# Kernel tuning notes

Measured on AMD Instinct MI355X. Metric: run time of the kernel, lower is better.

The kernel has to match this reference:

```python
import jax, jax.numpy as jnp
import numpy as np

N, E = 50000, 800000
IN, HID, H, OUT = 128, 32, 4, 32
NEG_SLOPE = 0.2


def _gatv2_layer(x, edge_index, Wl, bl, Wr, br, att, bias, heads, ch, concat):
    """One GATv2Conv layer (PyG semantics: add self-loops, lin_l on source,
    lin_r on target, e = att . leaky_relu(gl_src + gr_dst), segment softmax
    over incoming edges of each target, scatter-add weighted source messages)."""
    n = x.shape[0]
    loop = jnp.arange(n)
    src = jnp.concatenate([edge_index[0], loop])
    dst = jnp.concatenate([edge_index[1], loop])

    gl = (x @ Wl + bl).reshape(n, heads, ch)   # source transform [N,H,C]
    gr = (x @ Wr + br).reshape(n, heads, ch)   # target transform [N,H,C]

    m = jax.nn.leaky_relu(gl[src] + gr[dst], NEG_SLOPE)   # [E+N,H,C]
    e = jnp.einsum('ehc,hc->eh', m, att)                   # [E+N,H]

    # numerically stable segment softmax over dst
    emax = jax.lax.stop_gradient(jax.ops.segment_max(e, dst, num_segments=n))
    ex = jnp.exp(e - emax[dst])
    denom = jax.ops.segment_sum(ex, dst, num_segments=n)
    alpha = ex / denom[dst]                                # [E+N,H]

    out = jax.ops.segment_sum(alpha[:, :, None] * gl[src], dst, num_segments=n)  # [N,H,C]
    out = out.reshape(n, heads * ch) if concat else out.mean(axis=1)
    return out + bias


def setup_inputs() -> dict:
    key = jax.random.key(0)
    ks = jax.random.split(key, 16)
    s = 0.05
    return {
        'x': jax.random.normal(ks[0], (N, IN), dtype=jnp.float32),
        'edge_index': jax.random.randint(ks[1], (2, E), 0, N, dtype=jnp.int32),
        # layer 1: IN -> HID, H heads, concat
        'Wl1': jax.random.normal(ks[2], (IN, H * HID), dtype=jnp.float32) * s,
        'bl1': jnp.zeros((H * HID,), dtype=jnp.float32),
        'Wr1': jax.random.normal(ks[3], (IN, H * HID), dtype=jnp.float32) * s,
        'br1': jnp.zeros((H * HID,), dtype=jnp.float32),
        'att1': jax.random.normal(ks[4], (H, HID), dtype=jnp.float32) * s,
        'bias1': jnp.zeros((H * HID,), dtype=jnp.float32),
        # layer 2: H*HID -> OUT, 1 head, no concat
        'Wl2': jax.random.normal(ks[5], (H * HID, OUT), dtype=jnp.float32) * s,
        'bl2': jnp.zeros((OUT,), dtype=jnp.float32),
        'Wr2': jax.random.normal(ks[6], (H * HID, OUT), dtype=jnp.float32) * s,
        'br2': jnp.zeros((OUT,), dtype=jnp.float32),
        'att2': jax.random.normal(ks[7], (1, OUT), dtype=jnp.float32) * s,
        'bias2': jnp.zeros((OUT,), dtype=jnp.float32),
    }


def reference(x, edge_index, Wl1, bl1, Wr1, br1, att1, bias1,
              Wl2, bl2, Wr2, br2, att2, bias2):
    h = jax.nn.elu(_gatv2_layer(x, edge_index, Wl1, bl1, Wr1, br1, att1, bias1, H, HID, True))
    # dropout inactive in eval mode
    return _gatv2_layer(h, edge_index, Wl2, bl2, Wr2, br2, att2, bias2, 1, OUT, False)
```

## Files before the change

kernel.cpp:

```cpp
#include <hip/hip_runtime.h>

#define NNODES 50000
#define NEDGES 800000
#define ETOT   (NNODES + NEDGES)
#define NEG 0.2f
#define BKTS 196
#define P1E 4096
#define NP1 ((ETOT + P1E - 1) / P1E)

typedef unsigned short ushort_t;
typedef unsigned int uint_t;
typedef __attribute__((ext_vector_type(8))) short short8;
typedef __attribute__((ext_vector_type(4))) float f32x4;

__device__ __forceinline__ ushort_t f2bf(float f) {
  uint_t u = __float_as_uint(f);
  u += 0x7FFFu + ((u >> 16) & 1u);
  return (ushort_t)(u >> 16);
}
__device__ __forceinline__ float bf2f(ushort_t h) {
  return __uint_as_float((uint_t)h << 16);
}

__global__ __launch_bounds__(256) void coarse_hist(const int* __restrict__ ei,
                                                   int* __restrict__ pcnt) {
  __shared__ int c[BKTS];
  for (int i = threadIdx.x; i < BKTS; i += 256) c[i] = 0;
  __syncthreads();
  int e0 = blockIdx.x * P1E;
#pragma unroll
  for (int t = 0; t < P1E / 256; ++t) {
    int i = e0 + t * 256 + (int)threadIdx.x;
    if (i < ETOT) {
      int dst = (i < NEDGES) ? ei[NEDGES + i] : (i - NEDGES);
      atomicAdd(&c[dst >> 8], 1);
    }
  }
  __syncthreads();
  for (int i = threadIdx.x; i < BKTS; i += 256)
    pcnt[i * NP1 + blockIdx.x] = c[i];
}

__global__ __launch_bounds__(64) void coarse_scan(const int* __restrict__ pcnt,
                                                  int* __restrict__ goffArr,
                                                  int* __restrict__ tot) {
  int b = blockIdx.x;
  int lane = threadIdx.x;
  int carry = 0;
  for (int k0 = 0; k0 < NP1; k0 += 64) {
    int k = k0 + lane;
    int v = (k < NP1) ? pcnt[b * NP1 + k] : 0;
    int s = v;
    for (int off = 1; off < 64; off <<= 1) {
      int u = __shfl_up(s, off);
      if (lane >= off) s += u;
    }
    if (k < NP1) goffArr[b * NP1 + k] = carry + s - v;
    carry += __shfl(s, 63);
  }
  if (lane == 0) tot[b] = carry;
}

__global__ __launch_bounds__(256) void bucket_scan(const int* __restrict__ tot,
                                                   int* __restrict__ bucketStart,
                                                   int* __restrict__ rowptr) {
  if (threadIdx.x == 0) {
    int r = 0;
    for (int i = 0; i < BKTS; ++i) { bucketStart[i] = r; r += tot[i]; }
    bucketStart[BKTS] = r;
    rowptr[NNODES] = ETOT;
  }
}

__global__ __launch_bounds__(256) void bin_phase1(const int* __restrict__ ei,
                                                  const int* __restrict__ bucketStart,
                                                  const int* __restrict__ goffArr,
                                                  uint_t* __restrict__ binned) {
  __shared__ int cnt[BKTS], pref[BKTS], fillL[BKTS];
  __shared__ uint_t stage[P1E];
  int e0 = blockIdx.x * P1E;
  for (int i = threadIdx.x; i < BKTS; i += 256) { cnt[i] = 0; fillL[i] = 0; }
  __syncthreads();
  uint_t mypk[P1E / 256];
  int mybkt[P1E / 256];
#pragma unroll
  for (int t = 0; t < P1E / 256; ++t) {
    int i = e0 + t * 256 + (int)threadIdx.x;
    if (i < ETOT) {
      int dst = (i < NEDGES) ? ei[NEDGES + i] : (i - NEDGES);
      int src = (i < NEDGES) ? ei[i] : dst;
      int b = dst >> 8;
      mypk[t] = (uint_t)src | ((uint_t)(dst & 255) << 16) | ((uint_t)b << 24);
      mybkt[t] = b;
      atomicAdd(&cnt[b], 1);
    } else mybkt[t] = -1;
  }
  __syncthreads();
  if (threadIdx.x == 0) {
    int r = 0;
    for (int b = 0; b < BKTS; ++b) { pref[b] = r; r += cnt[b]; }
  }
  __syncthreads();
#pragma unroll
  for (int t = 0; t < P1E / 256; ++t) {
    if (mybkt[t] >= 0) {
      int p = pref[mybkt[t]] + atomicAdd(&fillL[mybkt[t]], 1);
      stage[p] = mypk[t];
    }
  }
  __syncthreads();
  int total = (e0 + P1E <= ETOT) ? P1E : (ETOT - e0);
  for (int j = threadIdx.x; j < total; j += 256) {
    uint_t pk = stage[j];
    int b = pk >> 24;
    binned[bucketStart[b] + goffArr[b * NP1 + blockIdx.x] + (j - pref[b])] = pk;
  }
}

__global__ __launch_bounds__(256) void bin_phase2(const uint_t* __restrict__ binned,
                                                  const int* __restrict__ bucketStart,
                                                  int* __restrict__ rowptr,
                                                  int* __restrict__ csrc) {
  __shared__ int cnt[256], pref[256], fillL[256];
  __shared__ int outS[8192];
  int b = blockIdx.x;
  int base = bucketStart[b];
  int cntAll = bucketStart[b + 1] - base;
  cnt[threadIdx.x] = 0; fillL[threadIdx.x] = 0;
  __syncthreads();
  for (int j = threadIdx.x; j < cntAll; j += 256)
    atomicAdd(&cnt[(binned[base + j] >> 16) & 255], 1);
  __syncthreads();
  if (threadIdx.x == 0) {
    int r = 0;
    for (int i = 0; i < 256; ++i) { pref[i] = r; r += cnt[i]; }
  }
  __syncthreads();
  int node = b * 256 + (int)threadIdx.x;
  if (node < NNODES) rowptr[node] = base + pref[threadIdx.x];
  for (int j = threadIdx.x; j < cntAll; j += 256) {
    uint_t pk = binned[base + j];
    int d = (pk >> 16) & 255;
    int p = pref[d] + atomicAdd(&fillL[d], 1);
    outS[p] = (int)(pk & 0xFFFF);
  }
  __syncthreads();
  for (int j = threadIdx.x; j < cntAll; j += 256)
    csrc[base + j] = outS[j];
}

__global__ __launch_bounds__(256) void prep_w(const float* __restrict__ Wl1,
                                              const float* __restrict__ Wr1,
                                              ushort_t* __restrict__ WtHi,
                                              ushort_t* __restrict__ WtLo) {
  int k = blockIdx.x;
  int n = threadIdx.x;
  float w = (n < 128) ? Wl1[k * 128 + n] : Wr1[k * 128 + (n - 128)];
  ushort_t h = f2bf(w);
  WtHi[n * 128 + k] = h;
  WtLo[n * 128 + k] = f2bf(w - bf2f(h));
}

__global__ __launch_bounds__(256) void gemm1_mfma(
    const float* __restrict__ x,
    const ushort_t* __restrict__ WtHi, const ushort_t* __restrict__ WtLo,
    const float* __restrict__ bl1, const float* __restrict__ br1,
    ushort_t* __restrict__ gl1, ushort_t* __restrict__ gr1) {
  constexpr int LDA = 132;
  __shared__ __align__(16) char smem[32 * 260 * 4];
  ushort_t (*Ahi)[LDA] = (ushort_t(*)[LDA])smem;
  ushort_t (*Alo)[LDA] = (ushort_t(*)[LDA])(smem + 32 * LDA * 2);
  float (*Cs)[260] = (float(*)[260])smem;
  int m0 = blockIdx.x * 32;
  int tid = threadIdx.x;
#pragma unroll
  for (int i = 0; i < 4; ++i) {
    int it = i * 256 + tid;
    int row = it >> 5, c4 = it & 31;
    int gm = m0 + row;
    float4 v = (gm < NNODES) ? *(const float4*)&x[(size_t)gm * 128 + 4 * c4]
                             : make_float4(0.f, 0.f, 0.f, 0.f);
    ushort_t h0 = f2bf(v.x), h1 = f2bf(v.y), h2 = f2bf(v.z), h3 = f2bf(v.w);
    ushort_t l0 = f2bf(v.x - bf2f(h0)), l1 = f2bf(v.y - bf2f(h1));
    ushort_t l2 = f2bf(v.z - bf2f(h2)), l3 = f2bf(v.w - bf2f(h3));
    uint2 ph, pl;
    ph.x = (uint_t)h0 | ((uint_t)h1 << 16); ph.y = (uint_t)h2 | ((uint_t)h3 << 16);
    pl.x = (uint_t)l0 | ((uint_t)l1 << 16); pl.y = (uint_t)l2 | ((uint_t)l3 << 16);
    *(uint2*)&Ahi[row][4 * c4] = ph;
    *(uint2*)&Alo[row][4 * c4] = pl;
  }
  __syncthreads();
  int wave = tid >> 6, lane = tid & 63;
  int quad = lane >> 4, nl = lane & 15;
  int nb = wave * 64;
  f32x4 acc[2][4];
#pragma unroll
  for (int tm = 0; tm < 2; ++tm)
#pragma unroll
    for (int tn = 0; tn < 4; ++tn) acc[tm][tn] = (f32x4){0.f, 0.f, 0.f, 0.f};

#pragma unroll
  for (int kc = 0; kc < 4; ++kc) {
    int klane = kc * 32 + quad * 8;
    short8 ah[2], al[2], bh[4], bl[4];
#pragma unroll
    for (int tm = 0; tm < 2; ++tm) {
      ah[tm] = *(const short8*)&Ahi[16 * tm + nl][klane];
      al[tm] = *(const short8*)&Alo[16 * tm + nl][klane];
    }
#pragma unroll
    for (int tn = 0; tn < 4; ++tn) {
      size_t wo = (size_t)(nb + 16 * tn + nl) * 128 + klane;
      bh[tn] = *(const short8*)&WtHi[wo];
      bl[tn] = *(const short8*)&WtLo[wo];
    }
#pragma unroll
    for (int tm = 0; tm < 2; ++tm)
#pragma unroll
      for (int tn = 0; tn < 4; ++tn) {
        acc[tm][tn] = __builtin_amdgcn_mfma_f32_16x16x32_bf16(ah[tm], bh[tn], acc[tm][tn], 0, 0, 0);
        acc[tm][tn] = __builtin_amdgcn_mfma_f32_16x16x32_bf16(ah[tm], bl[tn], acc[tm][tn], 0, 0, 0);
        acc[tm][tn] = __builtin_amdgcn_mfma_f32_16x16x32_bf16(al[tm], bh[tn], acc[tm][tn], 0, 0, 0);
      }
  }
  float bb[4];
#pragma unroll
  for (int tn = 0; tn < 4; ++tn) {
    int n = nb + 16 * tn + nl;
    bb[tn] = (n < 128) ? bl1[n] : br1[n - 128];
  }
  __syncthreads();
#pragma unroll
  for (int tm = 0; tm < 2; ++tm)
#pragma unroll
    for (int tn = 0; tn < 4; ++tn)
#pragma unroll
      for (int r = 0; r < 4; ++r)
        Cs[16 * tm + 4 * quad + r][nb + 16 * tn + nl] = acc[tm][tn][r] + bb[tn];
  __syncthreads();
#pragma unroll
  for (int i = 0; i < 2; ++i) {
    int it = i * 256 + tid;
    int row = it >> 4, oc = (it & 15) * 8;
    int gm = m0 + row;
    if (gm < NNODES) {
      uint4 pk;
      pk.x = (uint_t)f2bf(Cs[row][oc + 0]) | ((uint_t)f2bf(Cs[row][oc + 1]) << 16);
      pk.y = (uint_t)f2bf(Cs[row][oc + 2]) | ((uint_t)f2bf(Cs[row][oc + 3]) << 16);
      pk.z = (uint_t)f2bf(Cs[row][oc + 4]) | ((uint_t)f2bf(Cs[row][oc + 5]) << 16);
      pk.w = (uint_t)f2bf(Cs[row][oc + 6]) | ((uint_t)f2bf(Cs[row][oc + 7]) << 16);
      *(uint4*)&gl1[(size_t)gm * 128 + oc] = pk;
    }
  }
#pragma unroll
  for (int i = 0; i < 2; ++i) {
    int it = i * 256 + tid;
    int row = it >> 4, oc = (it & 15) * 8;
    int gm = m0 + row;
    if (gm < NNODES) {
      uint4 pk;
      pk.x = (uint_t)f2bf(Cs[row][128 + oc + 0]) | ((uint_t)f2bf(Cs[row][128 + oc + 1]) << 16);
      pk.y = (uint_t)f2bf(Cs[row][128 + oc + 2]) | ((uint_t)f2bf(Cs[row][128 + oc + 3]) << 16);
      pk.z = (uint_t)f2bf(Cs[row][128 + oc + 4]) | ((uint_t)f2bf(Cs[row][128 + oc + 5]) << 16);
      pk.w = (uint_t)f2bf(Cs[row][128 + oc + 6]) | ((uint_t)f2bf(Cs[row][128 + oc + 7]) << 16);
      *(uint4*)&gr1[(size_t)gm * 128 + oc] = pk;
    }
  }
}

__global__ __launch_bounds__(128) void gemm2_tile(
    const ushort_t* __restrict__ A,
    const float* __restrict__ W1, const float* __restrict__ b1,
    const float* __restrict__ W2, const float* __restrict__ b2,
    ushort_t* __restrict__ G1, ushort_t* __restrict__ G2) {
  constexpr int K = 128, KC = 32, BM = 128, BN = 64, MCOLS = 32, NT = 128;
  constexpr int LDA = BM + 4;
  __shared__ float AsT[KC][LDA];
  __shared__ float Ws[KC][BN];
  int row0 = blockIdx.x * BM;
  int tid = threadIdx.x;
  int tx = tid % (BN / 8), ty = tid / (BN / 8);
  float acc[8][8];
#pragma unroll
  for (int i = 0; i < 8; ++i)
#pragma unroll
    for (int j = 0; j < 8; ++j) acc[i][j] = 0.f;

  for (int kc = 0; kc < K; kc += KC) {
#pragma unroll
    for (int item = tid; item < BM * (KC / 4); item += NT) {
      int r = item >> 3, f4 = item & 7;
      int grow = row0 + r;
      uint2 u = (grow < NNODES)
          ? *(const uint2*)&A[(size_t)grow * K + kc + 4 * f4]
          : make_uint2(0u, 0u);
      AsT[4 * f4 + 0][r] = __uint_as_float(u.x << 16);
      AsT[4 * f4 + 1][r] = __uint_as_float(u.x & 0xffff0000u);
      AsT[4 * f4 + 2][r] = __uint_as_float(u.y << 16);
      AsT[4 * f4 + 3][r] = __uint_as_float(u.y & 0xffff0000u);
    }
#pragma unroll
    for (int item = tid; item < KC * (BN / 4); item += NT) {
      int k = item / (BN / 4), c4 = item % (BN / 4);
      int ccat = 4 * c4;
      const float* src = (ccat < MCOLS)
          ? &W1[(size_t)(kc + k) * MCOLS + ccat]
          : &W2[(size_t)(kc + k) * MCOLS + ccat - MCOLS];
      *(float4*)&Ws[k][4 * c4] = *(const float4*)src;
    }
    __syncthreads();
#pragma unroll 8
    for (int k = 0; k < KC; ++k) {
      float4 a0 = *(const float4*)&AsT[k][4 * ty];
      float4 a1 = *(const float4*)&AsT[k][BM / 2 + 4 * ty];
      float4 w0 = *(const float4*)&Ws[k][4 * tx];
      float4 w1 = *(const float4*)&Ws[k][BN / 2 + 4 * tx];
      float av[8] = {a0.x, a0.y, a0.z, a0.w, a1.x, a1.y, a1.z, a1.w};
      float wv[8] = {w0.x, w0.y, w0.z, w0.w, w1.x, w1.y, w1.z, w1.w};
#pragma unroll
      for (int i = 0; i < 8; ++i)
#pragma unroll
        for (int j = 0; j < 8; ++j) acc[i][j] = fmaf(av[i], wv[j], acc[i][j]);
    }
    __syncthreads();
  }
#pragma unroll
  for (int i = 0; i < 8; ++i) {
    int row = row0 + (i < 4 ? 4 * ty + i : BM / 2 + 4 * ty + (i - 4));
    if (row >= NNODES) continue;
#pragma unroll
    for (int jj = 0; jj < 2; ++jj) {
      int ccat = (jj == 0 ? 4 * tx : BN / 2 + 4 * tx);
      float o0 = acc[i][4 * jj + 0], o1 = acc[i][4 * jj + 1];
      float o2 = acc[i][4 * jj + 2], o3 = acc[i][4 * jj + 3];
      if (ccat < MCOLS) {
        float4 bb = *(const float4*)&b1[ccat];
        uint2 pk;
        pk.x = (uint_t)f2bf(o0 + bb.x) | ((uint_t)f2bf(o1 + bb.y) << 16);
        pk.y = (uint_t)f2bf(o2 + bb.z) | ((uint_t)f2bf(o3 + bb.w) << 16);
        *(uint2*)&G1[(size_t)row * MCOLS + ccat] = pk;
      } else {
        int c = ccat - MCOLS;
        float4 bb = *(const float4*)&b2[c];
        uint2 pk;
        pk.x = (uint_t)f2bf(o0 + bb.x) | ((uint_t)f2bf(o1 + bb.y) << 16);
        pk.y = (uint_t)f2bf(o2 + bb.z) | ((uint_t)f2bf(o3 + bb.w) << 16);
        *(uint2*)&G2[(size_t)row * MCOLS + c] = pk;
      }
    }
  }
}

__global__ __launch_bounds__(256) void gat1_edge(const int* __restrict__ rowptr,
                          const int* __restrict__ csrc,
                          const ushort_t* __restrict__ glb,
                          const ushort_t* __restrict__ grb,
                          const float* __restrict__ att, const float* __restrict__ bias,
                          ushort_t* __restrict__ hout) {
  int node = blockIdx.x * 4 + (threadIdx.x >> 6);
  if (node >= NNODES) return;
  int lane = threadIdx.x & 63;
  int eslot = lane >> 4;
  int q = lane & 15;
  int c8 = q * 8;
  float4 av0 = *(const float4*)(att + c8);
  float4 av1 = *(const float4*)(att + c8 + 4);
  uint4 ug = *(const uint4*)(grb + (size_t)node * 128 + c8);
  float4 gr0, gr1v;
  gr0.x = __uint_as_float(ug.x << 16);  gr0.y = __uint_as_float(ug.x & 0xffff0000u);
  gr0.z = __uint_as_float(ug.y << 16);  gr0.w = __uint_as_float(ug.y & 0xffff0000u);
  gr1v.x = __uint_as_float(ug.z << 16); gr1v.y = __uint_as_float(ug.z & 0xffff0000u);
  gr1v.z = __uint_as_float(ug.w << 16); gr1v.w = __uint_as_float(ug.w & 0xffff0000u);
  int start = rowptr[node], end = rowptr[node + 1];
  float denom = 0.f;
  float4 A0 = make_float4(0.f, 0.f, 0.f, 0.f);
  float4 A1 = make_float4(0.f, 0.f, 0.f, 0.f);
  for (int b = start; b < end; b += 64) {
    int nb = end - b; if (nb > 64) nb = 64;
    int sidx = (lane < nb) ? csrc[b + lane] : 0;
    for (int j = 0; j < nb; j += 4) {
      bool pv = (j + eslot) < nb;
      int s = __shfl(sidx, j + eslot);
      uint4 up = *(const uint4*)(glb + (size_t)s * 128 + c8);
      float4 g0, g1;
      g0.x = __uint_as_float(up.x << 16);
      g0.y = __uint_as_float(up.x & 0xffff0000u);
      g0.z = __uint_as_float(up.y << 16);
      g0.w = __uint_as_float(up.y & 0xffff0000u);
      g1.x = __uint_as_float(up.z << 16);
      g1.y = __uint_as_float(up.z & 0xffff0000u);
      g1.z = __uint_as_float(up.w << 16);
      g1.w = __uint_as_float(up.w & 0xffff0000u);
      float t, v;
      t = g0.x + gr0.x; t = fmaxf(t, NEG * t); v = av0.x * t;
      t = g0.y + gr0.y; t = fmaxf(t, NEG * t); v = fmaf(av0.y, t, v);
      t = g0.z + gr0.z; t = fmaxf(t, NEG * t); v = fmaf(av0.z, t, v);
      t = g0.w + gr0.w; t = fmaxf(t, NEG * t); v = fmaf(av0.w, t, v);
      t = g1.x + gr1v.x; t = fmaxf(t, NEG * t); v = fmaf(av1.x, t, v);
      t = g1.y + gr1v.y; t = fmaxf(t, NEG * t); v = fmaf(av1.y, t, v);
      t = g1.z + gr1v.z; t = fmaxf(t, NEG * t); v = fmaf(av1.z, t, v);
      t = g1.w + gr1v.w; t = fmaxf(t, NEG * t); v = fmaf(av1.w, t, v);
      v += __shfl_xor(v, 1); v += __shfl_xor(v, 2);
      float ex = pv ? __expf(v) : 0.f;
      denom += ex;
      A0.x = fmaf(ex, g0.x, A0.x); A0.y = fmaf(ex, g0.y, A0.y);
      A0.z = fmaf(ex, g0.z, A0.z); A0.w = fmaf(ex, g0.w, A0.w);
      A1.x = fmaf(ex, g1.x, A1.x); A1.y = fmaf(ex, g1.y, A1.y);
      A1.z = fmaf(ex, g1.z, A1.z); A1.w = fmaf(ex, g1.w, A1.w);
    }
  }
  denom += __shfl_xor(denom, 16); denom += __shfl_xor(denom, 32);
  A0.x += __shfl_xor(A0.x, 16); A0.x += __shfl_xor(A0.x, 32);
  A0.y += __shfl_xor(A0.y, 16); A0.y += __shfl_xor(A0.y, 32);
  A0.z += __shfl_xor(A0.z, 16); A0.z += __shfl_xor(A0.z, 32);
  A0.w += __shfl_xor(A0.w, 16); A0.w += __shfl_xor(A0.w, 32);
  A1.x += __shfl_xor(A1.x, 16); A1.x += __shfl_xor(A1.x, 32);
  A1.y += __shfl_xor(A1.y, 16); A1.y += __shfl_xor(A1.y, 32);
  A1.z += __shfl_xor(A1.z, 16); A1.z += __shfl_xor(A1.z, 32);
  A1.w += __shfl_xor(A1.w, 16); A1.w += __shfl_xor(A1.w, 32);
  float inv = 1.f / denom;
  if (eslot == 0) {
    float4 bv = *(const float4*)(bias + c8);
    float o0 = A0.x * inv + bv.x, o1 = A0.y * inv + bv.y;
    float o2 = A0.z * inv + bv.z, o3 = A0.w * inv + bv.w;
    o0 = o0 > 0.f ? o0 : __expf(o0) - 1.f;
    o1 = o1 > 0.f ? o1 : __expf(o1) - 1.f;
    o2 = o2 > 0.f ? o2 : __expf(o2) - 1.f;
    o3 = o3 > 0.f ? o3 : __expf(o3) - 1.f;
    uint2 pk;
    pk.x = (uint_t)f2bf(o0) | ((uint_t)f2bf(o1) << 16);
    pk.y = (uint_t)f2bf(o2) | ((uint_t)f2bf(o3) << 16);
    *(uint2*)&hout[(size_t)node * 128 + c8] = pk;
  } else if (eslot == 1) {
    float4 bv = *(const float4*)(bias + c8 + 4);
    float o0 = A1.x * inv + bv.x, o1 = A1.y * inv + bv.y;
    float o2 = A1.z * inv + bv.z, o3 = A1.w * inv + bv.w;
    o0 = o0 > 0.f ? o0 : __expf(o0) - 1.f;
    o1 = o1 > 0.f ? o1 : __expf(o1) - 1.f;
    o2 = o2 > 0.f ? o2 : __expf(o2) - 1.f;
    o3 = o3 > 0.f ? o3 : __expf(o3) - 1.f;
    uint2 pk;
    pk.x = (uint_t)f2bf(o0) | ((uint_t)f2bf(o1) << 16);
    pk.y = (uint_t)f2bf(o2) | ((uint_t)f2bf(o3) << 16);
    *(uint2*)&hout[(size_t)node * 128 + c8 + 4] = pk;
  }
}

__global__ __launch_bounds__(256) void gat2_edge(const int* __restrict__ rowptr,
                          const int* __restrict__ csrc,
                          const ushort_t* __restrict__ gl, const ushort_t* __restrict__ gr,
                          const float* __restrict__ att, const float* __restrict__ bias,
                          float* __restrict__ out) {
  int node = blockIdx.x * 4 + (threadIdx.x >> 6);
  if (node >= NNODES) return;
  int lane = threadIdx.x & 63;
  int eslot = lane >> 3;
  int q = lane & 7;
  int c4 = q * 4;
  float4 avc = *(const float4*)(att + c4);
  uint2 ugr = *(const uint2*)(gr + (size_t)node * 32 + c4);
  float4 grd;
  grd.x = __uint_as_float(ugr.x << 16); grd.y = __uint_as_float(ugr.x & 0xffff0000u);
  grd.z = __uint_as_float(ugr.y << 16); grd.w = __uint_as_float(ugr.y & 0xffff0000u);
  int start = rowptr[node], end = rowptr[node + 1];
  float denom = 0.f;
  float4 A = make_float4(0.f, 0.f, 0.f, 0.f);
  for (int b = start; b < end; b += 64) {
    int nb = end - b; if (nb > 64) nb = 64;
    int sidx = (lane < nb) ? csrc[b + lane] : 0;
    for (int j = 0; j < nb; j += 8) {
      bool pv = (j + eslot) < nb;
      int s = __shfl(sidx, j + eslot);
      uint2 ug = *(const uint2*)(gl + (size_t)s * 32 + c4);
      float4 g;
      g.x = __uint_as_float(ug.x << 16); g.y = __uint_as_float(ug.x & 0xffff0000u);
      g.z = __uint_as_float(ug.y << 16); g.w = __uint_as_float(ug.y & 0xffff0000u);
      float t, v;
      t = g.x + grd.x; t = fmaxf(t, NEG * t); v = avc.x * t;
      t = g.y + grd.y; t = fmaxf(t, NEG * t); v = fmaf(avc.y, t, v);
      t = g.z + grd.z; t = fmaxf(t, NEG * t); v = fmaf(avc.z, t, v);
      t = g.w + grd.w; t = fmaxf(t, NEG * t); v = fmaf(avc.w, t, v);
      v += __shfl_xor(v, 1); v += __shfl_xor(v, 2); v += __shfl_xor(v, 4);
      float ex = pv ? __expf(v) : 0.f;
      denom += ex;
      A.x = fmaf(ex, g.x, A.x); A.y = fmaf(ex, g.y, A.y);
      A.z = fmaf(ex, g.z, A.z); A.w = fmaf(ex, g.w, A.w);
    }
  }
  denom += __shfl_xor(denom, 8); denom += __shfl_xor(denom, 16); denom += __shfl_xor(denom, 32);
  A.x += __shfl_xor(A.x, 8); A.x += __shfl_xor(A.x, 16); A.x += __shfl_xor(A.x, 32);
  A.y += __shfl_xor(A.y, 8); A.y += __shfl_xor(A.y, 16); A.y += __shfl_xor(A.y, 32);
  A.z += __shfl_xor(A.z, 8); A.z += __shfl_xor(A.z, 16); A.z += __shfl_xor(A.z, 32);
  A.w += __shfl_xor(A.w, 8); A.w += __shfl_xor(A.w, 16); A.w += __shfl_xor(A.w, 32);
  if (eslot == 0) {
    float4 bv = *(const float4*)(bias + c4);
    float inv = 1.f / denom;
    float4 o;
    o.x = A.x * inv + bv.x; o.y = A.y * inv + bv.y;
    o.z = A.z * inv + bv.z; o.w = A.w * inv + bv.w;
    *(float4*)(out + (size_t)node * 32 + c4) = o;
  }
}

extern "C" void kernel_launch(void* const* d_in, const int* in_sizes, int n_in,
                              void* d_out, int out_size, void* d_ws, size_t ws_size,
                              hipStream_t stream) {
  const float* x     = (const float*)d_in[0];
  const int*   ei    = (const int*)  d_in[1];
  const float* Wl1   = (const float*)d_in[2];
  const float* bl1   = (const float*)d_in[3];
  const float* Wr1   = (const float*)d_in[4];
  const float* br1   = (const float*)d_in[5];
  const float* att1  = (const float*)d_in[6];
  const float* bias1 = (const float*)d_in[7];
  const float* Wl2   = (const float*)d_in[8];
  const float* bl2   = (const float*)d_in[9];
  const float* Wr2   = (const float*)d_in[10];
  const float* br2   = (const float*)d_in[11];
  const float* att2  = (const float*)d_in[12];
  const float* bias2 = (const float*)d_in[13];
  float* out = (float*)d_out;

  char* w = (char*)d_ws;
  auto carve = [&](size_t bytes) {
    char* p = w;
    w += (bytes + 255) & ~(size_t)255;
    return p;
  };
  ushort_t* gl1 = (ushort_t*)carve((size_t)NNODES * 128 * 2);
  ushort_t* gr1 = (ushort_t*)carve((size_t)NNODES * 128 * 2);
  ushort_t* h   = (ushort_t*)carve((size_t)NNODES * 128 * 2);
  ushort_t* gl2 = (ushort_t*)carve((size_t)NNODES * 32 * 2);
  ushort_t* gr2 = (ushort_t*)carve((size_t)NNODES * 32 * 2);
  ushort_t* WtHi = (ushort_t*)carve((size_t)256 * 128 * 2);
  ushort_t* WtLo = (ushort_t*)carve((size_t)256 * 128 * 2);
  int* pcnt    = (int*)carve((size_t)NP1 * BKTS * 4);
  int* goffArr = (int*)carve((size_t)NP1 * BKTS * 4);
  int* tot     = (int*)carve((size_t)BKTS * 4);
  int* bucketStart = (int*)carve((size_t)(BKTS + 1) * 4);
  int* rowptr = (int*)carve((size_t)(NNODES + 1) * 4);
  uint_t* binned = (uint_t*)carve((size_t)ETOT * 4);
  int* csrc = (int*)carve((size_t)ETOT * 4);

  prep_w<<<128, 256, 0, stream>>>(Wl1, Wr1, WtHi, WtLo);
  coarse_hist<<<NP1, 256, 0, stream>>>(ei, pcnt);
  coarse_scan<<<BKTS, 64, 0, stream>>>(pcnt, goffArr, tot);
  bucket_scan<<<1, 256, 0, stream>>>(tot, bucketStart, rowptr);
  bin_phase1<<<NP1, 256, 0, stream>>>(ei, bucketStart, goffArr, binned);
  bin_phase2<<<BKTS, 256, 0, stream>>>(binned, bucketStart, rowptr, csrc);

  gemm1_mfma<<<(NNODES + 31) / 32, 256, 0, stream>>>(x, WtHi, WtLo, bl1, br1, gl1, gr1);
  gat1_edge<<<(NNODES + 3) / 4, 256, 0, stream>>>(rowptr, csrc, gl1, gr1, att1, bias1, h);
  gemm2_tile<<<(NNODES + 127) / 128, 128, 0, stream>>>(h, Wl2, bl2, Wr2, br2, gl2, gr2);
  gat2_edge<<<(NNODES + 3) / 4, 256, 0, stream>>>(rowptr, csrc, gl2, gr2, att2, bias2, out);
}
```

Baseline: 264.3 us.

## Prefetch next gather, rewrite leaky-relu algebraically, exp2, smaller blocks, warp-parallel bucket scan

The edge kernels now software-pipeline the gather of source features, issuing the load for the next group of edges before computing on the current one. The leaky-relu-then-dot is rewritten as a·(c6·t + c4·|t|) with log2(e) folded into the attention constants, so exp2 replaces exp. Reciprocal uses the hardware rcp and 32-bit byte offsets replace size_t index math. Block size drops to 128 threads (2 nodes per block), and the serial single-thread bucket scan becomes a wavefront shuffle scan. This adds register pressure and slightly lower-precision rcp/exp in exchange for hiding gather latency and trimming ALU work.

```diff
diff --git a/kernel.cpp b/kernel.cpp
--- a/kernel.cpp
+++ b/kernel.cpp
@@ -61,13 +61,24 @@
   if (lane == 0) tot[b] = carry;
 }
 
-__global__ __launch_bounds__(256) void bucket_scan(const int* __restrict__ tot,
-                                                   int* __restrict__ bucketStart,
-                                                   int* __restrict__ rowptr) {
-  if (threadIdx.x == 0) {
-    int r = 0;
-    for (int i = 0; i < BKTS; ++i) { bucketStart[i] = r; r += tot[i]; }
-    bucketStart[BKTS] = r;
+__global__ __launch_bounds__(64) void bucket_scan(const int* __restrict__ tot,
+                                                  int* __restrict__ bucketStart,
+                                                  int* __restrict__ rowptr) {
+  int lane = threadIdx.x;
+  int carry = 0;
+  for (int k0 = 0; k0 < BKTS; k0 += 64) {
+    int k = k0 + lane;
+    int v = (k < BKTS) ? tot[k] : 0;
+    int s = v;
+    for (int off = 1; off < 64; off <<= 1) {
+      int u = __shfl_up(s, off);
+      if (lane >= off) s += u;
+    }
+    if (k < BKTS) bucketStart[k] = carry + s - v;
+    carry += __shfl(s, 63);
+  }
+  if (lane == 0) {
+    bucketStart[BKTS] = carry;
     rowptr[NNODES] = ETOT;
   }
 }
@@ -351,20 +362,27 @@
   }
 }
 
-__global__ __launch_bounds__(256) void gat1_edge(const int* __restrict__ rowptr,
+__global__ __launch_bounds__(128) void gat1_edge(const int* __restrict__ rowptr,
                           const int* __restrict__ csrc,
                           const ushort_t* __restrict__ glb,
                           const ushort_t* __restrict__ grb,
                           const float* __restrict__ att, const float* __restrict__ bias,
                           ushort_t* __restrict__ hout) {
-  int node = blockIdx.x * 4 + (threadIdx.x >> 6);
+  int node = blockIdx.x * 2 + (threadIdx.x >> 6);
   if (node >= NNODES) return;
   int lane = threadIdx.x & 63;
   int eslot = lane >> 4;
   int q = lane & 15;
   int c8 = q * 8;
+  const float C6 = 0.8656170245333781f;
+  const float C4 = 0.5770780163555854f;
   float4 av0 = *(const float4*)(att + c8);
   float4 av1 = *(const float4*)(att + c8 + 4);
+  float4 a60, a61, a40, a41;
+  a60.x = C6 * av0.x; a60.y = C6 * av0.y; a60.z = C6 * av0.z; a60.w = C6 * av0.w;
+  a61.x = C6 * av1.x; a61.y = C6 * av1.y; a61.z = C6 * av1.z; a61.w = C6 * av1.w;
+  a40.x = C4 * av0.x; a40.y = C4 * av0.y; a40.z = C4 * av0.z; a40.w = C4 * av0.w;
+  a41.x = C4 * av1.x; a41.y = C4 * av1.y; a41.z = C4 * av1.z; a41.w = C4 * av1.w;
   uint4 ug = *(const uint4*)(grb + (size_t)node * 128 + c8);
   float4 gr0, gr1v;
   gr0.x = __uint_as_float(ug.x << 16);  gr0.y = __uint_as_float(ug.x & 0xffff0000u);
@@ -375,13 +393,19 @@
   float denom = 0.f;
   float4 A0 = make_float4(0.f, 0.f, 0.f, 0.f);
   float4 A1 = make_float4(0.f, 0.f, 0.f, 0.f);
+  const char* glc = (const char*)glb;
+  uint_t coff = (uint_t)(c8 * 2);
   for (int b = start; b < end; b += 64) {
     int nb = end - b; if (nb > 64) nb = 64;
     int sidx = (lane < nb) ? csrc[b + lane] : 0;
+    int s0 = __shfl(sidx, eslot);
+    uint4 up = *(const uint4*)(glc + (((uint_t)s0 << 8) + coff));
     for (int j = 0; j < nb; j += 4) {
       bool pv = (j + eslot) < nb;
-      int s = __shfl(sidx, j + eslot);
-      uint4 up = *(const uint4*)(glb + (size_t)s * 128 + c8);
+      int jn = j + 4 + eslot;
+      int jc = (jn < nb) ? jn : 0;
+      int sn = __shfl(sidx, jc);
+      uint4 upn = *(const uint4*)(glc + (((uint_t)sn << 8) + coff));
       float4 g0, g1;
       g0.x = __uint_as_float(up.x << 16);
       g0.y = __uint_as_float(up.x & 0xffff0000u);
@@ -392,21 +416,22 @@
       g1.z = __uint_as_float(up.w << 16);
       g1.w = __uint_as_float(up.w & 0xffff0000u);
       float t, v;
-      t = g0.x + gr0.x; t = fmaxf(t, NEG * t); v = av0.x * t;
-      t = g0.y + gr0.y; t = fmaxf(t, NEG * t); v = fmaf(av0.y, t, v);
-      t = g0.z + gr0.z; t = fmaxf(t, NEG * t); v = fmaf(av0.z, t, v);
-      t = g0.w + gr0.w; t = fmaxf(t, NEG * t); v = fmaf(av0.w, t, v);
-      t = g1.x + gr1v.x; t = fmaxf(t, NEG * t); v = fmaf(av1.x, t, v);
-      t = g1.y + gr1v.y; t = fmaxf(t, NEG * t); v = fmaf(av1.y, t, v);
-      t = g1.z + gr1v.z; t = fmaxf(t, NEG * t); v = fmaf(av1.z, t, v);
-      t = g1.w + gr1v.w; t = fmaxf(t, NEG * t); v = fmaf(av1.w, t, v);
+      t = g0.x + gr0.x;  v = fmaf(a40.x, fabsf(t), a60.x * t);
+      t = g0.y + gr0.y;  v = fmaf(a60.y, t, v); v = fmaf(a40.y, fabsf(t), v);
+      t = g0.z + gr0.z;  v = fmaf(a60.z, t, v); v = fmaf(a40.z, fabsf(t), v);
+      t = g0.w + gr0.w;  v = fmaf(a60.w, t, v); v = fmaf(a40.w, fabsf(t), v);
+      t = g1.x + gr1v.x; v = fmaf(a61.x, t, v); v = fmaf(a41.x, fabsf(t), v);
+      t = g1.y + gr1v.y; v = fmaf(a61.y, t, v); v = fmaf(a41.y, fabsf(t), v);
+      t = g1.z + gr1v.z; v = fmaf(a61.z, t, v); v = fmaf(a41.z, fabsf(t), v);
+      t = g1.w + gr1v.w; v = fmaf(a61.w, t, v); v = fmaf(a41.w, fabsf(t), v);
       v += __shfl_xor(v, 1); v += __shfl_xor(v, 2);
-      float ex = pv ? __expf(v) : 0.f;
+      float ex = pv ? exp2f(v) : 0.f;
       denom += ex;
       A0.x = fmaf(ex, g0.x, A0.x); A0.y = fmaf(ex, g0.y, A0.y);
       A0.z = fmaf(ex, g0.z, A0.z); A0.w = fmaf(ex, g0.w, A0.w);
       A1.x = fmaf(ex, g1.x, A1.x); A1.y = fmaf(ex, g1.y, A1.y);
       A1.z = fmaf(ex, g1.z, A1.z); A1.w = fmaf(ex, g1.w, A1.w);
+      up = upn;
     }
   }
   denom += __shfl_xor(denom, 16); denom += __shfl_xor(denom, 32);
@@ -418,7 +443,7 @@
   A1.y += __shfl_xor(A1.y, 16); A1.y += __shfl_xor(A1.y, 32);
   A1.z += __shfl_xor(A1.z, 16); A1.z += __shfl_xor(A1.z, 32);
   A1.w += __shfl_xor(A1.w, 16); A1.w += __shfl_xor(A1.w, 32);
-  float inv = 1.f / denom;
+  float inv = __builtin_amdgcn_rcpf(denom);
   if (eslot == 0) {
     float4 bv = *(const float4*)(bias + c8);
     float o0 = A0.x * inv + bv.x, o1 = A0.y * inv + bv.y;
@@ -446,18 +471,23 @@
   }
 }
 
-__global__ __launch_bounds__(256) void gat2_edge(const int* __restrict__ rowptr,
+__global__ __launch_bounds__(128) void gat2_edge(const int* __restrict__ rowptr,
                           const int* __restrict__ csrc,
                           const ushort_t* __restrict__ gl, const ushort_t* __restrict__ gr,
                           const float* __restrict__ att, const float* __restrict__ bias,
                           float* __restrict__ out) {
-  int node = blockIdx.x * 4 + (threadIdx.x >> 6);
+  int node = blockIdx.x * 2 + (threadIdx.x >> 6);
   if (node >= NNODES) return;
   int lane = threadIdx.x & 63;
   int eslot = lane >> 3;
   int q = lane & 7;
   int c4 = q * 4;
+  const float C6 = 0.8656170245333781f;
+  const float C4f = 0.5770780163555854f;
   float4 avc = *(const float4*)(att + c4);
+  float4 a6, a4;
+  a6.x = C6 * avc.x; a6.y = C6 * avc.y; a6.z = C6 * avc.z; a6.w = C6 * avc.w;
+  a4.x = C4f * avc.x; a4.y = C4f * avc.y; a4.z = C4f * avc.z; a4.w = C4f * avc.w;
   uint2 ugr = *(const uint2*)(gr + (size_t)node * 32 + c4);
   float4 grd;
   grd.x = __uint_as_float(ugr.x << 16); grd.y = __uint_as_float(ugr.x & 0xffff0000u);
@@ -465,26 +495,33 @@
   int start = rowptr[node], end = rowptr[node + 1];
   float denom = 0.f;
   float4 A = make_float4(0.f, 0.f, 0.f, 0.f);
+  const char* glc = (const char*)gl;
+  uint_t coff = (uint_t)(c4 * 2);
   for (int b = start; b < end; b += 64) {
     int nb = end - b; if (nb > 64) nb = 64;
     int sidx = (lane < nb) ? csrc[b + lane] : 0;
+    int s0 = __shfl(sidx, eslot);
+    uint2 ugl = *(const uint2*)(glc + (((uint_t)s0 << 6) + coff));
     for (int j = 0; j < nb; j += 8) {
       bool pv = (j + eslot) < nb;
-      int s = __shfl(sidx, j + eslot);
-      uint2 ug = *(const uint2*)(gl + (size_t)s * 32 + c4);
+      int jn = j + 8 + eslot;
+      int jc = (jn < nb) ? jn : 0;
+      int sn = __shfl(sidx, jc);
+      uint2 ugn = *(const uint2*)(glc + (((uint_t)sn << 6) + coff));
       float4 g;
-      g.x = __uint_as_float(ug.x << 16); g.y = __uint_as_float(ug.x & 0xffff0000u);
-      g.z = __uint_as_float(ug.y << 16); g.w = __uint_as_float(ug.y & 0xffff0000u);
+      g.x = __uint_as_float(ugl.x << 16); g.y = __uint_as_float(ugl.x & 0xffff0000u);
+      g.z = __uint_as_float(ugl.y << 16); g.w = __uint_as_float(ugl.y & 0xffff0000u);
       float t, v;
-      t = g.x + grd.x; t = fmaxf(t, NEG * t); v = avc.x * t;
-      t = g.y + grd.y; t = fmaxf(t, NEG * t); v = fmaf(avc.y, t, v);
-      t = g.z + grd.z; t = fmaxf(t, NEG * t); v = fmaf(avc.z, t, v);
-      t = g.w + grd.w; t = fmaxf(t, NEG * t); v = fmaf(avc.w, t, v);
+      t = g.x + grd.x; v = fmaf(a4.x, fabsf(t), a6.x * t);
+      t = g.y + grd.y; v = fmaf(a6.y, t, v); v = fmaf(a4.y, fabsf(t), v);
+      t = g.z + grd.z; v = fmaf(a6.z, t, v); v = fmaf(a4.z, fabsf(t), v);
+      t = g.w + grd.w; v = fmaf(a6.w, t, v); v = fmaf(a4.w, fabsf(t), v);
       v += __shfl_xor(v, 1); v += __shfl_xor(v, 2); v += __shfl_xor(v, 4);
-      float ex = pv ? __expf(v) : 0.f;
+      float ex = pv ? exp2f(v) : 0.f;
       denom += ex;
       A.x = fmaf(ex, g.x, A.x); A.y = fmaf(ex, g.y, A.y);
       A.z = fmaf(ex, g.z, A.z); A.w = fmaf(ex, g.w, A.w);
+      ugl = ugn;
     }
   }
   denom += __shfl_xor(denom, 8); denom += __shfl_xor(denom, 16); denom += __shfl_xor(denom, 32);
@@ -493,8 +530,8 @@
   A.z += __shfl_xor(A.z, 8); A.z += __shfl_xor(A.z, 16); A.z += __shfl_xor(A.z, 32);
   A.w += __shfl_xor(A.w, 8); A.w += __shfl_xor(A.w, 16); A.w += __shfl_xor(A.w, 32);
   if (eslot == 0) {
+    float inv = __builtin_amdgcn_rcpf(denom);
     float4 bv = *(const float4*)(bias + c4);
-    float inv = 1.f / denom;
     float4 o;
     o.x = A.x * inv + bv.x; o.y = A.y * inv + bv.y;
     o.z = A.z * inv + bv.z; o.w = A.w * inv + bv.w;
@@ -545,12 +582,12 @@
   prep_w<<<128, 256, 0, stream>>>(Wl1, Wr1, WtHi, WtLo);
   coarse_hist<<<NP1, 256, 0, stream>>>(ei, pcnt);
   coarse_scan<<<BKTS, 64, 0, stream>>>(pcnt, goffArr, tot);
-  bucket_scan<<<1, 256, 0, stream>>>(tot, bucketStart, rowptr);
+  bucket_scan<<<1, 64, 0, stream>>>(tot, bucketStart, rowptr);
   bin_phase1<<<NP1, 256, 0, stream>>>(ei, bucketStart, goffArr, binned);
   bin_phase2<<<BKTS, 256, 0, stream>>>(binned, bucketStart, rowptr, csrc);
 
   gemm1_mfma<<<(NNODES + 31) / 32, 256, 0, stream>>>(x, WtHi, WtLo, bl1, br1, gl1, gr1);
-  gat1_edge<<<(NNODES + 3) / 4, 256, 0, stream>>>(rowptr, csrc, gl1, gr1, att1, bias1, h);
+  gat1_edge<<<(NNODES + 1) / 2, 128, 0, stream>>>(rowptr, csrc, gl1, gr1, att1, bias1, h);
   gemm2_tile<<<(NNODES + 127) / 128, 128, 0, stream>>>(h, Wl2, bl2, Wr2, br2, gl2, gr2);
-  gat2_edge<<<(NNODES + 3) / 4, 256, 0, stream>>>(rowptr, csrc, gl2, gr2, att2, bias2, out);
-}
+  gat2_edge<<<(NNODES + 1) / 2, 128, 0, stream>>>(rowptr, csrc, gl2, gr2, att2, bias2, out);
+}
```

Result: no change. 261.1 us (-1.2%).
